# Kernel optimization log

Hardware: AMD Instinct MI355X
Metric: run time of the kernel (lower is better)

The kernel has to match this reference:

```python
import jax, jax.numpy as jnp
import numpy as np
from jax import lax

UNITS = 25
IN_DIM = 64
BATCH = 256
SEQ = 2048


def _dense_params(key, fan_in, fan_out, bias_ones=False, use_bias=True):
    kw, kb = jax.random.split(key)
    scale = 1.0 / np.sqrt(fan_in)
    W = (jax.random.normal(kw, (fan_in, fan_out)) * scale).astype(jnp.float32)
    if not use_bias:
        return W
    b = jnp.ones((fan_out,), jnp.float32) if bias_ones else jnp.zeros((fan_out,), jnp.float32)
    return W, b


def setup_inputs() -> dict:
    key = jax.random.key(0)
    keys = jax.random.split(key, 20)
    x = jax.random.normal(keys[0], (BATCH, SEQ, IN_DIM), dtype=jnp.float32)

    def layer_params(ks, in_dim):
        Wxi, bi = _dense_params(ks[0], in_dim, UNITS)
        Whi = _dense_params(ks[1], UNITS, UNITS, use_bias=False)
        Wxf, bf = _dense_params(ks[2], in_dim, UNITS, bias_ones=True)  # forget bias init ones
        Whf = _dense_params(ks[3], UNITS, UNITS, use_bias=False)
        Wxc, bc = _dense_params(ks[4], in_dim, UNITS)
        Whc = _dense_params(ks[5], UNITS, UNITS, use_bias=False)
        Wxo, bo = _dense_params(ks[6], in_dim, UNITS)
        Who = _dense_params(ks[7], UNITS, UNITS, use_bias=False)
        return Wxi, bi, Whi, Wxf, bf, Whf, Wxc, bc, Whc, Wxo, bo, Who

    l1 = layer_params(keys[1:9], IN_DIM)
    l2 = layer_params(keys[9:17], UNITS)
    Wout, bout = _dense_params(keys[17], UNITS, 1)

    names = ['Wxi', 'bi', 'Whi', 'Wxf', 'bf', 'Whf', 'Wxc', 'bc', 'Whc', 'Wxo', 'bo', 'Who']
    d = {'x': x, 'Wout': Wout, 'bout': bout}
    for n, v in zip(names, l1):
        d['l1_' + n] = v
    for n, v in zip(names, l2):
        d['l2_' + n] = v
    return d


def _lstm_layer(x, Wxi, bi, Whi, Wxf, bf, Whf, Wxc, bc, Whc, Wxo, bo, Who):
    # x: [B, T, D] -> hidden states [B, T, H]
    B = x.shape[0]
    H = Whi.shape[0]
    # Precompute all input projections in one batched GEMM pass (same math as per-step Dense)
    xi = x @ Wxi + bi   # [B,T,H]
    xf = x @ Wxf + bf
    xc = x @ Wxc + bc
    xo = x @ Wxo + bo
    xs = jnp.stack([xi, xf, xc, xo], axis=0)          # [4,B,T,H]
    xs = jnp.moveaxis(xs, 2, 0)                       # [T,4,B,H]

    def step(carry, x_t):
        h, c_prev = carry
        x_i, x_f, x_c, x_o = x_t[0], x_t[1], x_t[2], x_t[3]
        i = jax.nn.sigmoid(x_i + h @ Whi)
        f = jax.nn.sigmoid(x_f + h @ Whf)
        g = jnp.tanh(x_c + h @ Whc)
        c_next = g * i + f * c_prev
        o = jax.nn.sigmoid(x_o + h @ Who)
        h_next = o * jnp.tanh(c_next)
        return (h_next, c_next), h_next

    init = (jnp.zeros((B, H), x.dtype), jnp.zeros((B, H), x.dtype))
    _, hs = lax.scan(step, init, xs)                  # hs: [T,B,H]
    return jnp.swapaxes(hs, 0, 1)                     # [B,T,H]


def reference(x,
              l1_Wxi, l1_bi, l1_Whi, l1_Wxf, l1_bf, l1_Whf, l1_Wxc, l1_bc, l1_Whc, l1_Wxo, l1_bo, l1_Who,
              l2_Wxi, l2_bi, l2_Whi, l2_Wxf, l2_bf, l2_Whf, l2_Wxc, l2_bc, l2_Whc, l2_Wxo, l2_bo, l2_Who,
              Wout, bout):
    h1 = _lstm_layer(x, l1_Wxi, l1_bi, l1_Whi, l1_Wxf, l1_bf, l1_Whf,
                     l1_Wxc, l1_bc, l1_Whc, l1_Wxo, l1_bo, l1_Who)
    h2 = _lstm_layer(h1, l2_Wxi, l2_bi, l2_Whi, l2_Wxf, l2_bf, l2_Whf,
                     l2_Wxc, l2_bc, l2_Whc, l2_Wxo, l2_bo, l2_Who)
    return jax.nn.sigmoid(h2 @ Wout + bout)           # [B,T,1]
```

## Files before the change

kernel.cpp:

```cpp
#include <hip/hip_runtime.h>
#include <cstdint>
#include <cstddef>

#define UNITS 25
#define IN_DIM 64
#define BATCH 256
#define SEQ 2048
#define BT (BATCH * SEQ)
#define L2E 1.442695040888963f

typedef _Float16 h2t __attribute__((ext_vector_type(2)));

#define R13(M) M(0) M(1) M(2) M(3) M(4) M(5) M(6) M(7) M(8) M(9) M(10) M(11) M(12)

__device__ __forceinline__ unsigned pk16(float lo, float hi) {
    return __builtin_bit_cast(unsigned, __builtin_amdgcn_cvt_pkrtz(lo, hi));
}
__device__ __forceinline__ float lo16(unsigned u) {
    return (float)__builtin_bit_cast(h2t, u).x;
}
__device__ __forceinline__ float hi16(unsigned u) {
    return (float)__builtin_bit_cast(h2t, u).y;
}
__device__ __forceinline__ float fdot2_(unsigned w, unsigned h, float c) {
#if __has_builtin(__builtin_amdgcn_fdot2)
    return __builtin_amdgcn_fdot2(__builtin_bit_cast(h2t, w),
                                  __builtin_bit_cast(h2t, h), c, false);
#else
    h2t W = __builtin_bit_cast(h2t, w), H = __builtin_bit_cast(h2t, h);
    return fmaf((float)W.x, (float)H.x, fmaf((float)W.y, (float)H.y, c));
#endif
}
__device__ __forceinline__ float dswap(float v) {
    return __int_as_float(__builtin_amdgcn_mov_dpp(__float_as_int(v), 0xB1, 0xF, 0xF, true));
}
__device__ __forceinline__ float dpp2(float v) {
    return __int_as_float(__builtin_amdgcn_mov_dpp(__float_as_int(v), 0xAA, 0xF, 0xF, true));
}
__device__ __forceinline__ unsigned rdlu(unsigned v, int lane) {
    return (unsigned)__builtin_amdgcn_readlane((int)v, lane);
}
__device__ __forceinline__ float sig_raw(float a) {
    return __builtin_amdgcn_rcpf(1.0f + __builtin_amdgcn_exp2f(a));
}
__device__ __forceinline__ float tanh5(float c) {
    return fmaf(2.0f, __builtin_amdgcn_rcpf(
        1.0f + __builtin_amdgcn_exp2f(-2.0f * L2E * c)), -1.0f);
}
__device__ __forceinline__ unsigned ldpin(const unsigned* p) {
    unsigned v;
    asm volatile("global_load_dword %0, %1, off\n\ts_waitcnt vmcnt(0)"
                 : "=v"(v) : "v"(p) : "memory");
    return v;
}
__device__ __forceinline__ void wgbar() {
    asm volatile("s_waitcnt lgkmcnt(0)\n\ts_barrier" ::: "memory");
}


__device__ unsigned g_w1[13 * 100];
__device__ unsigned g_wx[13 * 100];
__device__ unsigned g_wh[13 * 100];
__device__ unsigned g_wo[13];
__device__ unsigned g_Wp16[100 * 32];
__device__ float    g_bp[100];

__global__ void prep_kernel(const float* __restrict__ l1_Whi, const float* __restrict__ l1_Whf,
                            const float* __restrict__ l1_Whc, const float* __restrict__ l1_Who,
                            const float* __restrict__ l1_Wxi, const float* __restrict__ l1_Wxf,
                            const float* __restrict__ l1_Wxc, const float* __restrict__ l1_Wxo,
                            const float* __restrict__ l1_bi,  const float* __restrict__ l1_bf,
                            const float* __restrict__ l1_bc,  const float* __restrict__ l1_bo,
                            const float* __restrict__ l2_Wxi, const float* __restrict__ l2_Wxf,
                            const float* __restrict__ l2_Wxc, const float* __restrict__ l2_Wxo,
                            const float* __restrict__ l2_Whi, const float* __restrict__ l2_Whf,
                            const float* __restrict__ l2_Whc, const float* __restrict__ l2_Who,
                            const float* __restrict__ Wout) {
    const int c = threadIdx.x;
    if (c < 100) {
        const int half = (c >= 50);
        const int l = half ? c - 50 : c;
        const int u = l >> 1;
        const int par = l & 1;
        const float s = (half && !par) ? (-2.0f * L2E) : (-L2E);
        const float* W1 = half ? (par ? l1_Who : l1_Whc) : (par ? l1_Whf : l1_Whi);
        const float* WX = half ? (par ? l2_Wxo : l2_Wxc) : (par ? l2_Wxf : l2_Wxi);
        const float* WH = half ? (par ? l2_Who : l2_Whc) : (par ? l2_Whf : l2_Whi);
        const float* WI = half ? (par ? l1_Wxo : l1_Wxc) : (par ? l1_Wxf : l1_Wxi);
        const float* bI = half ? (par ? l1_bo  : l1_bc)  : (par ? l1_bf  : l1_bi);
        for (int i = 0; i < 13; ++i) {
            const int k0 = 2 * i, k1 = 2 * i + 1;
            const float a1 = s * W1[k0 * UNITS + u];
            const float b1 = (k1 < UNITS) ? s * W1[k1 * UNITS + u] : 0.f;
            g_w1[i * 100 + c] = pk16(a1, b1);
            const float ax = s * WX[k0 * UNITS + u];
            const float bx = (k1 < UNITS) ? s * WX[k1 * UNITS + u] : 0.f;
            g_wx[i * 100 + c] = pk16(ax, bx);
            const float ah = s * WH[k0 * UNITS + u];
            const float bh = (k1 < UNITS) ? s * WH[k1 * UNITS + u] : 0.f;
            g_wh[i * 100 + c] = pk16(ah, bh);
        }
        for (int kp = 0; kp < 32; ++kp)
            g_Wp16[c * 32 + kp] = pk16(s * WI[(2 * kp) * UNITS + u],
                                       s * WI[(2 * kp + 1) * UNITS + u]);
        g_bp[c] = s * bI[u];
    }
    if (c == 100) {
        for (int i = 0; i < 13; ++i) {
            const int k1 = 2 * i + 1;
            g_wo[i] = pk16(Wout[2 * i], (k1 < UNITS) ? Wout[k1] : 0.f);
        }
    }
}

#define PCH 10
__global__ __launch_bounds__(256, 2)
void proj_kernel(const float* __restrict__ x, unsigned* __restrict__ pre2h) {
    __shared__ unsigned ob[2][256 * PCH];
    const int tid = threadIdx.x;
    const int r0 = blockIdx.x * 512 + tid;
    const int r1 = r0 + 256;

    uint4 xp[2][8];
    #pragma unroll
    for (int r = 0; r < 2; ++r) {
        const float4* xr = (const float4*)(x + (size_t)(r ? r1 : r0) * IN_DIM);
        #pragma unroll
        for (int j = 0; j < 8; ++j) {
            const float4 a = xr[2 * j], b = xr[2 * j + 1];
            xp[r][j] = make_uint4(pk16(a.x, a.y), pk16(a.z, a.w),
                                  pk16(b.x, b.y), pk16(b.z, b.w));
        }
    }

    #pragma unroll 1
    for (int ch = 0; ch < 50; ch += PCH) {
        #pragma unroll 1
        for (int cc = 0; cc < PCH; ++cc) {
            const int c = ch + cc;
            const uint4* wA = (const uint4*)(g_Wp16 + c * 32);
            const uint4* wB = (const uint4*)(g_Wp16 + (c + 50) * 32);
            float aA0 = g_bp[c],      aA1 = 0.f;
            float bA0 = 0.f, bA1 = 0.f;
            float aB0 = g_bp[c + 50], aB1 = 0.f, bB0 = 0.f, bB1 = 0.f;
            float cA0 = g_bp[c],      cA1 = 0.f, dA0 = 0.f, dA1 = 0.f;
            float cB0 = g_bp[c + 50], cB1 = 0.f, dB0 = 0.f, dB1 = 0.f;
            #pragma unroll
            for (int j = 0; j < 8; ++j) {
                const uint4 wa = wA[j], wb = wB[j];
                const uint4 x0 = xp[0][j], x1 = xp[1][j];
                aA0 = fdot2_(wa.x, x0.x, aA0); bA0 = fdot2_(wa.y, x0.y, bA0);
                aA1 = fdot2_(wa.z, x0.z, aA1); bA1 = fdot2_(wa.w, x0.w, bA1);
                aB0 = fdot2_(wb.x, x0.x, aB0); bB0 = fdot2_(wb.y, x0.y, bB0);
                aB1 = fdot2_(wb.z, x0.z, aB1); bB1 = fdot2_(wb.w, x0.w, bB1);
                cA0 = fdot2_(wa.x, x1.x, cA0); dA0 = fdot2_(wa.y, x1.y, dA0);
                cA1 = fdot2_(wa.z, x1.z, cA1); dA1 = fdot2_(wa.w, x1.w, dA1);
                cB0 = fdot2_(wb.x, x1.x, cB0); dB0 = fdot2_(wb.y, x1.y, dB0);
                cB1 = fdot2_(wb.z, x1.z, cB1); dB1 = fdot2_(wb.w, x1.w, dB1);
            }
            ob[0][tid * PCH + cc] = pk16((aA0 + aA1) + (bA0 + bA1),
                                         (aB0 + aB1) + (bB0 + bB1));
            ob[1][tid * PCH + cc] = pk16((cA0 + cA1) + (dA0 + dA1),
                                         (cB0 + cB1) + (dB0 + dB1));
        }
        __syncthreads();
        #pragma unroll
        for (int g = 0; g < 2; ++g) {
            const size_t rowbase = ((size_t)blockIdx.x * 512 + g * 256) * 50 + ch;
            #pragma unroll
            for (int k = 0; k < PCH; ++k) {
                const int i = tid + k * 256;
                const int row = i / PCH;
                const int c2 = i - row * PCH;
                pre2h[rowbase + (size_t)row * 50 + c2] = ob[g][i];
            }
        }
        __syncthreads();
    }
}

template<bool HOFF>
__global__ __attribute__((amdgpu_waves_per_eu(1, 1))) __launch_bounds__(128)
void lstm_scan_kernel(const unsigned* __restrict__ pre2h,
                      const float* __restrict__ l2_bi, const float* __restrict__ l2_bf,
                      const float* __restrict__ l2_bc, const float* __restrict__ l2_bo,
                      const float* __restrict__ bout,
                      float* __restrict__ h2buf, float* __restrict__ out) {
    __shared__ float2 xsl[2][4][64];
    const int tid = threadIdx.x;
    const int l   = tid & 63;
    const int b   = blockIdx.x;
    const int lc  = (l < 50) ? l : 49;
    const int uu  = lc >> 1;
    const bool odd = (l & 1);
    const float tA = odd ? 1.0f : 2.0f;
    const float tC = odd ? 0.0f : -1.0f;

    if (tid < 64) {
        const float b2A = (odd ? l2_bf[uu] : l2_bi[uu]) * (-L2E);
        const float b2B = odd ? (l2_bo[uu] * (-L2E)) : (l2_bc[uu] * (-2.0f * L2E));
        #define LW(i) const unsigned w1A_##i = ldpin(g_w1 + (i)*100 + lc);      \
                      const unsigned w1B_##i = ldpin(g_w1 + (i)*100 + 50 + lc); \
                      const unsigned wxA_##i = ldpin(g_wx + (i)*100 + lc);      \
                      const unsigned wxB_##i = ldpin(g_wx + (i)*100 + 50 + lc);
        R13(LW)
        #undef LW
        #define DH(i) unsigned s1_##i = 0u;
        R13(DH)
        #undef DH
        float c1 = 0.f;

        const unsigned* prow = pre2h + (size_t)b * SEQ * 50 + lc;
        const unsigned p0 = prow[0];
        float aA = lo16(p0), aB = hi16(p0);
        unsigned q1 = prow[50], q2 = prow[100], q3 = prow[150];

        auto stepA = [&](unsigned pw, float2* xs) {
            const float avA = sig_raw(aA);
            const float avB = fmaf(tA, sig_raw(aB), tC);
            const float fv = dswap(avA);
            const float ov = dswap(avB);
            c1 = fmaf(avB, avA, fv * c1);
            const float h1v = ov * tanh5(c1);
            const unsigned m1 = pk16(h1v, dpp2(h1v));
            #define BC1(i) s1_##i = rdlu(m1, 4 * (i));
            R13(BC1)
            #undef BC1
            float naA = lo16(pw), naB = hi16(pw);
            float xA = b2A, xB = b2B;
            #define DD(i) xA  = fdot2_(wxA_##i, s1_##i, xA);  \
                          xB  = fdot2_(wxB_##i, s1_##i, xB);  \
                          naA = fdot2_(w1A_##i, s1_##i, naA); \
                          naB = fdot2_(w1B_##i, s1_##i, naB);
            R13(DD)
            #undef DD
            xs[l] = make_float2(xA, xB);
            aA = naA; aB = naB;
        };

        #pragma unroll 1
        for (int g = 0; g < SEQ / 4; ++g) {
            const int rb = (g < SEQ / 4 - 1) ? 4 * (g + 1) : (SEQ - 4);
            const unsigned* pg = prow + (size_t)rb * 50;
            const unsigned n0 = pg[0], n1 = pg[50], n2 = pg[100], n3 = pg[150];
            float2* xs = &xsl[g & 1][0][0];
            stepA(q1, xs);
            stepA(q2, xs + 64);
            stepA(q3, xs + 128);
            stepA(n0, xs + 192);
            q1 = n1; q2 = n2; q3 = n3;
            wgbar();
        }
    } else {
        const float boutv = HOFF ? 0.f : bout[0];
        #define LW(i) const unsigned whA_##i = ldpin(g_wh + (i)*100 + lc);      \
                      const unsigned whB_##i = ldpin(g_wh + (i)*100 + 50 + lc);
        R13(LW)
        #undef LW
        #define LWO(i) const unsigned wo_##i = HOFF ? 0u : g_wo[i];
        R13(LWO)
        #undef LWO
        #define DH(i) unsigned s2_##i = 0u;
        R13(DH)
        #undef DH
        float c2 = 0.f;
        float* h2p = HOFF ? (h2buf + (size_t)b * SEQ * UNITS + uu) : nullptr;
        const bool st = (l < 50) && !odd;

        auto stepB = [&](int t, float2 xv) {
            float hA0 = 0.f, hA1 = 0.f, hB0 = 0.f, hB1 = 0.f;
            #define D0(i) hA0 = fdot2_(whA_##i, s2_##i, hA0); \
                          hB0 = fdot2_(whB_##i, s2_##i, hB0);
            #define D1(i) hA1 = fdot2_(whA_##i, s2_##i, hA1); \
                          hB1 = fdot2_(whB_##i, s2_##i, hB1);
            D0(0) D1(1) D0(2) D1(3) D0(4) D1(5) D0(6)
            D1(7) D0(8) D1(9) D0(10) D1(11) D0(12)
            #undef D0
            #undef D1
            const float avA2 = sig_raw(xv.x + (hA0 + hA1));
            const float avB2 = fmaf(tA, sig_raw(xv.y + (hB0 + hB1)), tC);
            const float fv2 = dswap(avA2);
            const float ov2 = dswap(avB2);
            c2 = fmaf(avB2, avA2, fv2 * c2);
            const float h2v = ov2 * tanh5(c2);
            if (HOFF) {
                if (st) h2p[(size_t)t * UNITS] = h2v;
            }
            const unsigned m2 = pk16(h2v, dpp2(h2v));
            #define BC2(i) s2_##i = rdlu(m2, 4 * (i));
            R13(BC2)
            #undef BC2
            if (!HOFF) {
                float hp = boutv;
                #define HH(i) hp = fdot2_(wo_##i, s2_##i, hp);
                R13(HH)
                #undef HH
                if (l == 0) out[(size_t)b * SEQ + t] = sig_raw(-L2E * hp);
            }
        };

        #pragma unroll 1
        for (int g = 0; g < SEQ / 4; ++g) {
            wgbar();
            const float2* xs = &xsl[g & 1][0][0];
            const float2 xv0 = xs[lc];
            const float2 xv1 = xs[64 + lc];
            const float2 xv2 = xs[128 + lc];
            const float2 xv3 = xs[192 + lc];
            const int t = 4 * g;
            stepB(t,     xv0);
            stepB(t + 1, xv1);
            stepB(t + 2, xv2);
            stepB(t + 3, xv3);
        }
    }
}

__global__ __launch_bounds__(256)
void head_kernel(const float* __restrict__ h2buf, const float* __restrict__ Wout,
                 const float* __restrict__ bout, float* __restrict__ out) {
    __shared__ float wl[26];
    if (threadIdx.x < 25) wl[threadIdx.x] = Wout[threadIdx.x];
    if (threadIdx.x == 25) wl[25] = bout[0];
    __syncthreads();
    const int r = blockIdx.x * 256 + threadIdx.x;
    const float* hp = h2buf + (size_t)r * UNITS;
    float p0 = wl[25], p1 = 0.f;
    #pragma unroll
    for (int k = 0; k < UNITS; ++k) {
        if (k & 1) p1 = fmaf(hp[k], wl[k], p1);
        else       p0 = fmaf(hp[k], wl[k], p0);
    }
    out[r] = sig_raw(-L2E * (p0 + p1));
}

extern "C" void kernel_launch(void* const* d_in, const int* in_sizes, int n_in,
                              void* d_out, int out_size, void* d_ws, size_t ws_size,
                              hipStream_t stream) {
    const float* x      = (const float*)d_in[0];
    const float* Wout   = (const float*)d_in[1];
    const float* bout   = (const float*)d_in[2];
    const float* l1_Wxi = (const float*)d_in[3];
    const float* l1_bi  = (const float*)d_in[4];
    const float* l1_Whi = (const float*)d_in[5];
    const float* l1_Wxf = (const float*)d_in[6];
    const float* l1_bf  = (const float*)d_in[7];
    const float* l1_Whf = (const float*)d_in[8];
    const float* l1_Wxc = (const float*)d_in[9];
    const float* l1_bc  = (const float*)d_in[10];
    const float* l1_Whc = (const float*)d_in[11];
    const float* l1_Wxo = (const float*)d_in[12];
    const float* l1_bo  = (const float*)d_in[13];
    const float* l1_Who = (const float*)d_in[14];
    const float* l2_Wxi = (const float*)d_in[15];
    const float* l2_bi  = (const float*)d_in[16];
    const float* l2_Whi = (const float*)d_in[17];
    const float* l2_Wxf = (const float*)d_in[18];
    const float* l2_bf  = (const float*)d_in[19];
    const float* l2_Whf = (const float*)d_in[20];
    const float* l2_Wxc = (const float*)d_in[21];
    const float* l2_bc  = (const float*)d_in[22];
    const float* l2_Whc = (const float*)d_in[23];
    const float* l2_Wxo = (const float*)d_in[24];
    const float* l2_bo  = (const float*)d_in[25];
    const float* l2_Who = (const float*)d_in[26];
    float* out = (float*)d_out;

    const size_t pre_bytes = (size_t)BT * 50 * sizeof(unsigned);
    const size_t h2_bytes  = (size_t)BT * UNITS * sizeof(float);
    unsigned* pre2h = (unsigned*)d_ws;

    prep_kernel<<<1, 128, 0, stream>>>(
        l1_Whi, l1_Whf, l1_Whc, l1_Who,
        l1_Wxi, l1_Wxf, l1_Wxc, l1_Wxo,
        l1_bi, l1_bf, l1_bc, l1_bo,
        l2_Wxi, l2_Wxf, l2_Wxc, l2_Wxo,
        l2_Whi, l2_Whf, l2_Whc, l2_Who,
        Wout);
    proj_kernel<<<BT / 512, 256, 0, stream>>>(x, pre2h);

    if (ws_size >= pre_bytes + h2_bytes) {
        float* h2buf = (float*)((char*)d_ws + pre_bytes);
        lstm_scan_kernel<true><<<BATCH, 128, 0, stream>>>(
            pre2h, l2_bi, l2_bf, l2_bc, l2_bo, bout, h2buf, out);
        head_kernel<<<BT / 256, 256, 0, stream>>>(h2buf, Wout, bout, out);
    } else {
        lstm_scan_kernel<false><<<BATCH, 128, 0, stream>>>(
            pre2h, l2_bi, l2_bf, l2_bc, l2_bo, bout, nullptr, out);
    }
}
```

Baseline: 748.7 us.

## Rewrite input projection kernel with MFMA 16x16x32 f16 tiles

Replaces the per-thread fdot2 input projection with an MFMA-based GEMM. Each block stages 64 rows of x and the packed weights in LDS, computes 100 output columns with mfma_f32_16x16x32_f16, then adds bias and writes packed f16 pairs. This targets the ALU-bound dot-product work in the projection stage, at the cost of more blocks, extra LDS staging and padded wasted columns. The end-to-end effect depends on how much of the total time the projection accounts for compared with the sequential scan.

Result: faster. 699.7 us (-6.5%).

```diff
diff --git a/kernel.cpp b/kernel.cpp
--- a/kernel.cpp
+++ b/kernel.cpp
@@ -10,6 +10,8 @@
 #define L2E 1.442695040888963f
 
 typedef _Float16 h2t __attribute__((ext_vector_type(2)));
+typedef _Float16 f16x8 __attribute__((ext_vector_type(8)));
+typedef float f32x4 __attribute__((ext_vector_type(4)));
 
 #define R13(M) M(0) M(1) M(2) M(3) M(4) M(5) M(6) M(7) M(8) M(9) M(10) M(11) M(12)
 
@@ -113,69 +115,64 @@
     }
 }
 
-#define PCH 10
-__global__ __launch_bounds__(256, 2)
+__global__ __launch_bounds__(256)
 void proj_kernel(const float* __restrict__ x, unsigned* __restrict__ pre2h) {
-    __shared__ unsigned ob[2][256 * PCH];
+    __shared__ unsigned xs[64 * 36];
+    __shared__ unsigned wls[100 * 36];
+    __shared__ float bls[100];
+    __shared__ float of32[64 * 112];
     const int tid = threadIdx.x;
-    const int r0 = blockIdx.x * 512 + tid;
-    const int r1 = r0 + 256;
-
-    uint4 xp[2][8];
+
+    for (int i = tid; i < 3200; i += 256)
+        wls[(i >> 5) * 36 + (i & 31)] = g_Wp16[i];
+    if (tid < 100) bls[tid] = g_bp[tid];
+
+    const float4* xg = (const float4*)(x + (size_t)blockIdx.x * 64 * IN_DIM);
     #pragma unroll
-    for (int r = 0; r < 2; ++r) {
-        const float4* xr = (const float4*)(x + (size_t)(r ? r1 : r0) * IN_DIM);
-        #pragma unroll
-        for (int j = 0; j < 8; ++j) {
-            const float4 a = xr[2 * j], b = xr[2 * j + 1];
-            xp[r][j] = make_uint4(pk16(a.x, a.y), pk16(a.z, a.w),
-                                  pk16(b.x, b.y), pk16(b.z, b.w));
-        }
-    }
-
-    #pragma unroll 1
-    for (int ch = 0; ch < 50; ch += PCH) {
-        #pragma unroll 1
-        for (int cc = 0; cc < PCH; ++cc) {
-            const int c = ch + cc;
-            const uint4* wA = (const uint4*)(g_Wp16 + c * 32);
-            const uint4* wB = (const uint4*)(g_Wp16 + (c + 50) * 32);
-            float aA0 = g_bp[c],      aA1 = 0.f;
-            float bA0 = 0.f, bA1 = 0.f;
-            float aB0 = g_bp[c + 50], aB1 = 0.f, bB0 = 0.f, bB1 = 0.f;
-            float cA0 = g_bp[c],      cA1 = 0.f, dA0 = 0.f, dA1 = 0.f;
-            float cB0 = g_bp[c + 50], cB1 = 0.f, dB0 = 0.f, dB1 = 0.f;
+    for (int k = 0; k < 4; ++k) {
+        const int q = tid + (k << 8);
+        const float4 a = xg[q];
+        const int row = q >> 4;
+        const int fc = q & 15;
+        *(uint2*)&xs[row * 36 + 2 * fc] = make_uint2(pk16(a.x, a.y), pk16(a.z, a.w));
+    }
+    __syncthreads();
+
+    const int w = tid >> 6, l = tid & 63;
+    const int lr = l & 15, lg = l >> 4;
+    const unsigned* xrow = xs + (16 * w + lr) * 36;
+    const f16x8 a0 = __builtin_bit_cast(f16x8, *(const uint4*)(xrow + 4 * lg));
+    const f16x8 a1 = __builtin_bit_cast(f16x8, *(const uint4*)(xrow + 16 + 4 * lg));
+
+    #pragma unroll
+    for (int nt = 0; nt < 7; ++nt) {
+        const int c = nt * 16 + lr;
+        const int cl = (c < 100) ? c : 99;
+        const unsigned* wrow = wls + cl * 36;
+        const f16x8 b0 = __builtin_bit_cast(f16x8, *(const uint4*)(wrow + 4 * lg));
+        const f16x8 b1 = __builtin_bit_cast(f16x8, *(const uint4*)(wrow + 16 + 4 * lg));
+        f32x4 acc = {0.f, 0.f, 0.f, 0.f};
+        acc = __builtin_amdgcn_mfma_f32_16x16x32_f16(a0, b0, acc, 0, 0, 0);
+        acc = __builtin_amdgcn_mfma_f32_16x16x32_f16(a1, b1, acc, 0, 0, 0);
+        if (c < 100) {
             #pragma unroll
-            for (int j = 0; j < 8; ++j) {
-                const uint4 wa = wA[j], wb = wB[j];
-                const uint4 x0 = xp[0][j], x1 = xp[1][j];
-                aA0 = fdot2_(wa.x, x0.x, aA0); bA0 = fdot2_(wa.y, x0.y, bA0);
-                aA1 = fdot2_(wa.z, x0.z, aA1); bA1 = fdot2_(wa.w, x0.w, bA1);
-                aB0 = fdot2_(wb.x, x0.x, aB0); bB0 = fdot2_(wb.y, x0.y, bB0);
-                aB1 = fdot2_(wb.z, x0.z, aB1); bB1 = fdot2_(wb.w, x0.w, bB1);
-                cA0 = fdot2_(wa.x, x1.x, cA0); dA0 = fdot2_(wa.y, x1.y, dA0);
-                cA1 = fdot2_(wa.z, x1.z, cA1); dA1 = fdot2_(wa.w, x1.w, dA1);
-                cB0 = fdot2_(wb.x, x1.x, cB0); dB0 = fdot2_(wb.y, x1.y, dB0);
-                cB1 = fdot2_(wb.z, x1.z, cB1); dB1 = fdot2_(wb.w, x1.w, dB1);
-            }
-            ob[0][tid * PCH + cc] = pk16((aA0 + aA1) + (bA0 + bA1),
-                                         (aB0 + aB1) + (bB0 + bB1));
-            ob[1][tid * PCH + cc] = pk16((cA0 + cA1) + (dA0 + dA1),
-                                         (cB0 + cB1) + (dB0 + dB1));
-        }
-        __syncthreads();
-        #pragma unroll
-        for (int g = 0; g < 2; ++g) {
-            const size_t rowbase = ((size_t)blockIdx.x * 512 + g * 256) * 50 + ch;
-            #pragma unroll
-            for (int k = 0; k < PCH; ++k) {
-                const int i = tid + k * 256;
-                const int row = i / PCH;
-                const int c2 = i - row * PCH;
-                pre2h[rowbase + (size_t)row * 50 + c2] = ob[g][i];
-            }
-        }
-        __syncthreads();
+            for (int r = 0; r < 4; ++r)
+                of32[(16 * w + 4 * lg + r) * 112 + c] = acc[r];
+        }
+    }
+    __syncthreads();
+
+    const size_t base = (size_t)blockIdx.x * 64 * 50;
+    #pragma unroll
+    for (int k = 0; k < 13; ++k) {
+        const int i = tid + (k << 8);
+        if (i < 3200) {
+            const int row = i / 50;
+            const int d = i - row * 50;
+            const float pa = of32[row * 112 + d] + bls[d];
+            const float pb = of32[row * 112 + d + 50] + bls[d + 50];
+            pre2h[base + i] = pk16(pa, pb);
+        }
     }
 }
 
@@ -377,7 +374,7 @@
         l2_Wxi, l2_Wxf, l2_Wxc, l2_Wxo,
         l2_Whi, l2_Whf, l2_Whc, l2_Who,
         Wout);
-    proj_kernel<<<BT / 512, 256, 0, stream>>>(x, pre2h);
+    proj_kernel<<<BT / 64, 256, 0, stream>>>(x, pre2h);
 
     if (ws_size >= pre_bytes + h2_bytes) {
         float* h2buf = (float*)((char*)d_ws + pre_bytes);
```
